# Kernel tuning notes

Hardware: AMD Instinct MI355X
Metric: run time of the kernel (lower is better)

The kernel has to match this reference:

```python
import jax, jax.numpy as jnp
import numpy as np

B, C, H, W = 4, 256, 64, 64
CQK = C // 2


def setup_inputs() -> dict:
    key = jax.random.key(0)
    ks = jax.random.split(key, 8)
    s = 0.05
    return {
        "x": jax.random.normal(ks[0], (B, C, H, W), dtype=jnp.float32),
        "wq": jax.random.normal(ks[1], (CQK, C), dtype=jnp.float32) * s,
        "bq": jax.random.normal(ks[2], (CQK,), dtype=jnp.float32) * s,
        "wk": jax.random.normal(ks[3], (CQK, C), dtype=jnp.float32) * s,
        "bk": jax.random.normal(ks[4], (CQK,), dtype=jnp.float32) * s,
        "wv": jax.random.normal(ks[5], (C, C), dtype=jnp.float32) * s,
        "bv": jax.random.normal(ks[6], (C,), dtype=jnp.float32) * s,
        "gamma": jax.random.normal(ks[7], (1,), dtype=jnp.float32),
    }


def reference(x, wq, bq, wk, bk, wv, bv, gamma):
    b, c, h, w = x.shape
    n = h * w
    xf = x.reshape(b, c, n)  # [B,C,N]
    # 1x1 convs == per-pixel linear projections
    q = jnp.einsum("oc,bcn->bon", wq, xf) + bq[:, None]  # [B,C/2,N]
    k = jnp.einsum("oc,bcn->bon", wk, xf) + bk[:, None]  # [B,C/2,N]
    v = jnp.einsum("oc,bcn->bon", wv, xf) + bv[:, None]  # [B,C,N]
    # attention[b,m,n'] = softmax_n'( sum_d q[b,d,m] * k[b,d,n'] )
    scores = jnp.einsum("bdm,bdn->bmn", q, k)  # [B,N,N]
    attn = jax.nn.softmax(scores, axis=2)
    # out_feat[b,c,j] = sum_i v[b,c,i] * attn[b,i,j]  (matmul(value, attention))
    af = jnp.einsum("bci,bij->bcj", v, attn)  # [B,C,N]
    out = gamma[0] * af.reshape(b, c, h, w) + x
    return out
```

## Files before the change

### kernel.cpp

```cpp
#include <hip/hip_runtime.h>
#include <hip/hip_bf16.h>


typedef _Float16 f16;
typedef _Float16 f16x4v __attribute__((ext_vector_type(4)));
typedef _Float16 f16x8v __attribute__((ext_vector_type(8)));
typedef float f32x4v __attribute__((ext_vector_type(4)));

static __device__ __forceinline__ f32x4v mfma16(f16x8v a, f16x8v b, f32x4v c) {
  return __builtin_amdgcn_mfma_f32_16x16x32_f16(a, b, c, 0, 0, 0);
}

#define AS1q __attribute__((address_space(1)))
#define AS3q __attribute__((address_space(3)))
static __device__ __forceinline__ void gl_lds16(const void* g, void* l) {
  __builtin_amdgcn_global_load_lds((const AS1q unsigned int*)g,
                                   (AS3q unsigned int*)l, 16, 0, 0);
}

__global__ void k_wcvt(const float* __restrict__ wq, const float* __restrict__ bq,
                       const float* __restrict__ wk, const float* __restrict__ bk,
                       const float* __restrict__ wv, const float* __restrict__ bv,
                       f16* __restrict__ wh, float* __restrict__ bcat) {
  int o = blockIdx.x;
  int c = threadIdx.x;
  const float* wrow; float bias;
  if (o < 128)      { wrow = wq + (size_t)o * 256;         bias = bq[o]; }
  else if (o < 256) { wrow = wk + (size_t)(o - 128) * 256; bias = bk[o - 128]; }
  else              { wrow = wv + (size_t)(o - 256) * 256; bias = bv[o - 256]; }
  wh[(size_t)o * 256 + c] = (f16)wrow[c];
  if (c == 0) bcat[o] = bias;
}

__global__ void k_xsplit(const float* __restrict__ x, f16* __restrict__ xh) {
  __shared__ float t[64][65];
  int b = blockIdx.z, c0 = blockIdx.y * 64, n0 = blockIdx.x * 64;
  int tx = threadIdx.x & 63, ty = threadIdx.x >> 6;
  const float* xb = x + ((size_t)b * 256 + c0) * 4096 + n0;
#pragma unroll
  for (int r = ty; r < 64; r += 4) t[r][tx] = xb[(size_t)r * 4096 + tx];
  __syncthreads();
  f16* dh = xh + ((size_t)b * 4096 + n0) * 256 + c0;
#pragma unroll
  for (int r = ty; r < 64; r += 4)
    dh[(size_t)r * 256 + tx] = (f16)t[tx][r];
}

__global__ void __launch_bounds__(256, 2)
k_proj(const f16* __restrict__ xh, const f16* __restrict__ wh,
       const float* __restrict__ bcat, f16* __restrict__ qT,
       f16* __restrict__ kT, f16* __restrict__ vT) {
  extern __shared__ char smem[];
  int b = blockIdx.z, m0 = blockIdx.y * 64, n0 = blockIdx.x * 64;
  int tid = threadIdx.x, l = tid & 63, w = tid >> 6;
  int col = l & 15, quad = l >> 4;
  const f16* Ag = xh + ((size_t)b * 4096 + m0) * 256;
  const f16* Wg = wh + (size_t)n0 * 256;
  int rloc = l >> 5;
  int l5 = l & 31;
#pragma unroll
  for (int p = 0; p < 8; p++) {
    int ci = w * 8 + p;
    int r = ci * 2 + rloc;
    int g = l5 ^ (r & 31);
    gl_lds16(Ag + (size_t)r * 256 + g * 8, smem + ci * 1024);
    gl_lds16(Wg + (size_t)r * 256 + g * 8, smem + 32768 + ci * 1024);
  }
  __syncthreads();
  const char* sA = smem;
  const char* sW = smem + 32768;
  f32x4v acc[4] = {};
  int ar = w * 16 + col;
#pragma unroll
  for (int ks = 0; ks < 8; ks++) {
    int G = ks * 4 + quad;
    f16x8v a = *(const f16x8v*)(sA + ar * 512 + ((G ^ (ar & 31)) * 16));
#pragma unroll
    for (int nt = 0; nt < 4; nt++) {
      int wr = nt * 16 + col;
      f16x8v bb = *(const f16x8v*)(sW + wr * 512 + ((G ^ (wr & 31)) * 16));
      acc[nt] = mfma16(a, bb, acc[nt]);
    }
  }
  if (n0 < 256) {
#pragma unroll
    for (int nt = 0; nt < 4; nt++) {
      int o = n0 + nt * 16 + col;
      float bias = bcat[o];
      int d = o & 127;
      f16* dst = (o < 128) ? qT : kT;
      size_t tb = (size_t)b * 524288 + (size_t)(m0 / 16 + w) * 2048 +
                  (size_t)(d >> 5) * 512 + (size_t)((d >> 3) & 3) * 128 + (d & 7);
#pragma unroll
      for (int rg = 0; rg < 4; rg++)
        dst[tb + (quad * 4 + rg) * 8] = (f16)(acc[nt][rg] + bias);
    }
  } else {
    int i2 = w * 16 + quad * 4;
    int it2 = (m0 + i2) >> 5;
    int qd2 = (i2 >> 3) & 3;
    int e2 = i2 & 7;
#pragma unroll
    for (int nt = 0; nt < 4; nt++) {
      int o = n0 + nt * 16 + col;
      float bias = bcat[o];
      int c = o - 256;
      f16x4v pv;
#pragma unroll
      for (int rg = 0; rg < 4; rg++) pv[rg] = (f16)(acc[nt][rg] + bias);
      size_t addr = (size_t)b * 1048576 + (size_t)(c >> 4) * 65536 +
                    (size_t)it2 * 512 + (size_t)qd2 * 128 + (size_t)(c & 15) * 8 + e2;
      *(f16x4v*)&vT[addr] = pv;
    }
  }
}

__global__ void __launch_bounds__(512, 2)
k_rows(const f16* __restrict__ qT, const f16* __restrict__ kT,
       float* __restrict__ partial) {
  int jblk = blockIdx.x, ih = blockIdx.y, b = blockIdx.z;
  int tid = threadIdx.x, l = tid & 63, w = tid >> 6;
  int col = l & 15;
  int ti = w & 3, jh = w >> 2;
  const f16* ktb = kT + (size_t)b * 524288 + (size_t)(jblk * 8 + jh * 4) * 2048 + l * 8;
  const f16* qtb = qT + (size_t)b * 524288 + (size_t)ti * 2048 + l * 8;
  f16x8v ka[4][4];
#pragma unroll
  for (int jt = 0; jt < 4; jt++)
#pragma unroll
    for (int ks = 0; ks < 4; ks++)
      ka[jt][ks] = *(const f16x8v*)(ktb + jt * 2048 + ks * 512);
  float* pout = partial + ((size_t)(b * 32 + jblk) * 2 + jh) * 4096 + ti * 16 + col;
  int it0 = ih * 32;
  f16x8v qfA[4], qfB[4];
#pragma unroll
  for (int ks = 0; ks < 4; ks++)
    qfA[ks] = *(const f16x8v*)(qtb + (size_t)it0 * 8192 + ks * 512);

#define ROWS_BODY(IT, QF, QN, PREF)                                           \
  {                                                                           \
    if (PREF) {                                                               \
      _Pragma("unroll") for (int ks = 0; ks < 4; ks++)                        \
        QN[ks] = *(const f16x8v*)(qtb + (size_t)((IT) + 1) * 8192 + ks * 512);\
    }                                                                         \
    f32x4v s[4] = {};                                                         \
    _Pragma("unroll") for (int ks = 0; ks < 4; ks++) {                        \
      s[0] = mfma16(ka[0][ks], QF[ks], s[0]);                                 \
      s[1] = mfma16(ka[1][ks], QF[ks], s[1]);                                 \
      s[2] = mfma16(ka[2][ks], QF[ks], s[2]);                                 \
      s[3] = mfma16(ka[3][ks], QF[ks], s[3]);                                 \
    }                                                                         \
    float t = 0.f;                                                            \
    _Pragma("unroll") for (int jt = 0; jt < 4; jt++)                          \
      _Pragma("unroll") for (int rg = 0; rg < 4; rg++)                        \
        t += __expf(s[jt][rg]);                                               \
    t += __shfl_xor(t, 16);                                                   \
    t += __shfl_xor(t, 32);                                                   \
    if (l < 16) pout[(size_t)(IT) * 64] = t;                                  \
  }

  for (int itp = 0; itp < 16; itp++) {
    int itA = it0 + itp * 2;
    ROWS_BODY(itA, qfA, qfB, true)
    ROWS_BODY(itA + 1, qfB, qfA, itp < 15)
  }
#undef ROWS_BODY
}

__global__ void k_rsum(const float* __restrict__ partial, float* __restrict__ rinv) {
  int b = blockIdx.y;
  int i = blockIdx.x * 256 + threadIdx.x;
  const float* p = partial + (size_t)b * 64 * 4096 + i;
  float s = 0.f;
#pragma unroll 8
  for (int jb = 0; jb < 64; jb++) s += p[(size_t)jb * 4096];
  rinv[(size_t)b * 4096 + i] = 1.0f / s;
}

__global__ void __launch_bounds__(512, 2)
k_fav(const f16* __restrict__ qT, const f16* __restrict__ kT,
      const f16* __restrict__ vT, const float* __restrict__ rinv,
      const float* __restrict__ x, const float* __restrict__ gamma,
      float* __restrict__ out) {
  __shared__ f16 sE[2][4096];
  int wg = blockIdx.x;
  int lg = (wg & 7) * 32 + (wg >> 3);
  int b = lg >> 6, j0 = (lg & 63) * 64;
  int tid = threadIdx.x, l = tid & 63, w = tid >> 6;
  int col = l & 15, quad = l >> 4;
  int ti = w & 3, tjb = (w >> 2) * 2;
  const f16* ktb = kT + (size_t)b * 524288 + (size_t)(j0 / 16 + tjb) * 2048 + l * 8;
  const f16* qtb = qT + (size_t)b * 524288 + (size_t)ti * 2048 + l * 8;
  const f16* vtb = vT + (size_t)b * 1048576 + (size_t)(w * 2) * 65536 + l * 8;
  const float* rp = rinv + (size_t)b * 4096 + ti * 16 + col;
  f16x8v ka0[4], ka1[4];
#pragma unroll
  for (int ks = 0; ks < 4; ks++) {
    ka0[ks] = *(const f16x8v*)(ktb + ks * 512);
    ka1[ks] = *(const f16x8v*)(ktb + 2048 + ks * 512);
  }
  f16x8v qfA[4], qfB[4], vfA[2][2], vfB[2][2];
  float rvA, rvB;
#pragma unroll
  for (int ks = 0; ks < 4; ks++) qfA[ks] = *(const f16x8v*)(qtb + ks * 512);
#pragma unroll
  for (int mt = 0; mt < 2; mt++)
#pragma unroll
    for (int ks = 0; ks < 2; ks++)
      vfA[mt][ks] = *(const f16x8v*)(vtb + mt * 65536 + ks * 512);
  rvA = rp[0];
  f32x4v acc[2][4] = {};
  int ig = ti * 2 + (col >> 3);
  int i_lo = col & 7;

#define FAV_BODY(IT, QF, VF, RV, QN, VN, RN, PREF, SEB)                        \
  {                                                                            \
    if (PREF) {                                                                \
      _Pragma("unroll") for (int ks = 0; ks < 4; ks++)                         \
        QN[ks] = *(const f16x8v*)(qtb + (size_t)((IT) + 1) * 8192 + ks * 512); \
      _Pragma("unroll") for (int mt = 0; mt < 2; mt++)                         \
        _Pragma("unroll") for (int ks = 0; ks < 2; ks++)                       \
          VN[mt][ks] = *(const f16x8v*)(vtb + mt * 65536 +                     \
                                        (size_t)(((IT) + 1) * 2 + ks) * 512);  \
      RN = rp[((IT) + 1) * 64];                                                \
    }                                                                          \
    f32x4v s0 = {}, s1 = {};                                                   \
    _Pragma("unroll") for (int ks = 0; ks < 4; ks++) {                         \
      s0 = mfma16(ka0[ks], QF[ks], s0);                                        \
      s1 = mfma16(ka1[ks], QF[ks], s1);                                        \
    }                                                                          \
    _Pragma("unroll") for (int rg = 0; rg < 4; rg++) {                         \
      int jl0 = tjb * 16 + quad * 4 + rg;                                      \
      sE[SEB][jl0 * 64 + ((ig ^ (jl0 & 7)) * 8) + i_lo] = (f16)(__expf(s0[rg]) * RV); \
      sE[SEB][(jl0 + 16) * 64 + ((ig ^ (jl0 & 7)) * 8) + i_lo] = (f16)(__expf(s1[rg]) * RV); \
    }                                                                          \
    asm volatile("s_waitcnt lgkmcnt(0)\n\ts_barrier" ::: "memory");            \
    _Pragma("unroll") for (int ks = 0; ks < 2; ks++) {                         \
      int sw = ((ks * 4 + quad) ^ (col & 7)) * 8;                              \
      f16x8v e0 = *(const f16x8v*)&sE[SEB][col * 64 + sw];                     \
      f16x8v e1 = *(const f16x8v*)&sE[SEB][(16 + col) * 64 + sw];              \
      f16x8v e2 = *(const f16x8v*)&sE[SEB][(32 + col) * 64 + sw];              \
      f16x8v e3 = *(const f16x8v*)&sE[SEB][(48 + col) * 64 + sw];              \
      acc[0][0] = mfma16(VF[0][ks], e0, acc[0][0]);                            \
      acc[0][1] = mfma16(VF[0][ks], e1, acc[0][1]);                            \
      acc[0][2] = mfma16(VF[0][ks], e2, acc[0][2]);                            \
      acc[0][3] = mfma16(VF[0][ks], e3, acc[0][3]);                            \
      acc[1][0] = mfma16(VF[1][ks], e0, acc[1][0]);                            \
      acc[1][1] = mfma16(VF[1][ks], e1, acc[1][1]);                            \
      acc[1][2] = mfma16(VF[1][ks], e2, acc[1][2]);                            \
      acc[1][3] = mfma16(VF[1][ks], e3, acc[1][3]);                            \
    }                                                                          \
  }

  for (int itp = 0; itp < 32; itp++) {
    int itA = itp * 2;
    FAV_BODY(itA, qfA, vfA, rvA, qfB, vfB, rvB, true, 0)
    FAV_BODY(itA + 1, qfB, vfB, rvB, qfA, vfA, rvA, itp < 31, 1)
  }
#undef FAV_BODY

  float gm = gamma[0];
  const float* xb = x + (size_t)b * 256 * 4096;
  float* ob = out + (size_t)b * 256 * 4096;
#pragma unroll
  for (int mt = 0; mt < 2; mt++)
#pragma unroll
    for (int jt = 0; jt < 4; jt++) {
      int c = w * 32 + mt * 16 + quad * 4;
      int j = j0 + jt * 16 + col;
#pragma unroll
      for (int rg = 0; rg < 4; rg++) {
        size_t off = (size_t)(c + rg) * 4096 + j;
        ob[off] = gm * acc[mt][jt][rg] + xb[off];
      }
    }
}

extern "C" void kernel_launch(void* const* d_in, const int* in_sizes, int n_in,
                              void* d_out, int out_size, void* d_ws, size_t ws_size,
                              hipStream_t stream) {
  (void)in_sizes; (void)n_in; (void)out_size; (void)ws_size;
  const float* x  = (const float*)d_in[0];
  const float* wq = (const float*)d_in[1];
  const float* bq = (const float*)d_in[2];
  const float* wk = (const float*)d_in[3];
  const float* bk = (const float*)d_in[4];
  const float* wv = (const float*)d_in[5];
  const float* bv = (const float*)d_in[6];
  const float* gm = (const float*)d_in[7];
  float* out = (float*)d_out;

  char* ws = (char*)d_ws;
  f16*  xh = (f16*)ws;
  f16*  qT = (f16*)(ws + 8388608);
  f16*  kT = (f16*)(ws + 12582912);
  f16*  vT = (f16*)(ws + 16777216);
  f16*  wh = (f16*)(ws + 25165824);
  float* bcat    = (float*)(ws + 25427968);
  float* rinv    = (float*)(ws + 25430016);
  float* partial = (float*)(ws + 25495552);

  hipLaunchKernelGGL(k_wcvt, dim3(512), dim3(256), 0, stream, wq, bq, wk, bk, wv, bv, wh, bcat);
  hipLaunchKernelGGL(k_xsplit, dim3(64, 4, 4), dim3(256), 0, stream, x, xh);
  hipLaunchKernelGGL(k_proj, dim3(8, 64, 4), dim3(256), 65536, stream, xh, wh, bcat, qT, kT, vT);
  hipLaunchKernelGGL(k_rows, dim3(32, 2, 4), dim3(512), 0, stream, qT, kT, partial);
  hipLaunchKernelGGL(k_rsum, dim3(16, 4), dim3(256), 0, stream, partial, rinv);
  hipLaunchKernelGGL(k_fav, dim3(256), dim3(512), 0, stream, qT, kT, vT, rinv, x, gm, out);
}
```

Baseline: 184.3 us.

## Pre-tile x and weights into MFMA fragment layout; register-resident projection GEMM

The weight-conversion and x-transpose kernels now write f16 data directly in the 16-row MFMA fragment-tiled layout, so each lane can load its operand fragments with contiguous 16-byte global loads. The projection kernel drops the LDS staging and swizzle. Each 512-thread block keeps its weight fragments in registers and loops over 8 token tiles, double-buffering the activation fragments with prefetch. This removes the LDS round-trip and reloading of weights per 64x64 tile. In exchange, the grid shrinks from 2048 to 256 blocks, and register pressure at launch bounds (512,1) is higher.

```diff
diff --git a/kernel.cpp b/kernel.cpp
--- a/kernel.cpp
+++ b/kernel.cpp
@@ -9,13 +9,6 @@
 
 static __device__ __forceinline__ f32x4v mfma16(f16x8v a, f16x8v b, f32x4v c) {
   return __builtin_amdgcn_mfma_f32_16x16x32_f16(a, b, c, 0, 0, 0);
-}
-
-#define AS1q __attribute__((address_space(1)))
-#define AS3q __attribute__((address_space(3)))
-static __device__ __forceinline__ void gl_lds16(const void* g, void* l) {
-  __builtin_amdgcn_global_load_lds((const AS1q unsigned int*)g,
-                                   (AS3q unsigned int*)l, 16, 0, 0);
 }
 
 __global__ void k_wcvt(const float* __restrict__ wq, const float* __restrict__ bq,
@@ -28,7 +21,8 @@
   if (o < 128)      { wrow = wq + (size_t)o * 256;         bias = bq[o]; }
   else if (o < 256) { wrow = wk + (size_t)(o - 128) * 256; bias = bk[o - 128]; }
   else              { wrow = wv + (size_t)(o - 256) * 256; bias = bv[o - 256]; }
-  wh[(size_t)o * 256 + c] = (f16)wrow[c];
+  wh[(size_t)(o >> 4) * 4096 + (size_t)(c >> 5) * 512 +
+     (size_t)((c >> 3) & 3) * 128 + (o & 15) * 8 + (c & 7)] = (f16)wrow[c];
   if (c == 0) bcat[o] = bias;
 }
 
@@ -40,79 +34,94 @@
 #pragma unroll
   for (int r = ty; r < 64; r += 4) t[r][tx] = xb[(size_t)r * 4096 + tx];
   __syncthreads();
-  f16* dh = xh + ((size_t)b * 4096 + n0) * 256 + c0;
-#pragma unroll
-  for (int r = ty; r < 64; r += 4)
-    dh[(size_t)r * 256 + tx] = (f16)t[tx][r];
-}
-
-__global__ void __launch_bounds__(256, 2)
+  f16* xbb = xh + (size_t)b * 1048576;
+#pragma unroll
+  for (int k2 = 0; k2 < 2; k2++) {
+    int id = k2 * 256 + threadIdx.x;
+    int tok = id & 63, oct = id >> 6;
+    int tt = n0 + tok;
+    f16x8v v;
+#pragma unroll
+    for (int e = 0; e < 8; e++) v[e] = (f16)t[oct * 8 + e][tok];
+    size_t addr = (size_t)(tt >> 4) * 4096 +
+                  (size_t)((c0 >> 5) + (oct >> 2)) * 512 +
+                  (size_t)(oct & 3) * 128 + (tt & 15) * 8;
+    *(f16x8v*)&xbb[addr] = v;
+  }
+}
+
+__global__ void __launch_bounds__(512, 1)
 k_proj(const f16* __restrict__ xh, const f16* __restrict__ wh,
        const float* __restrict__ bcat, f16* __restrict__ qT,
        f16* __restrict__ kT, f16* __restrict__ vT) {
-  extern __shared__ char smem[];
-  int b = blockIdx.z, m0 = blockIdx.y * 64, n0 = blockIdx.x * 64;
+  int ob = blockIdx.x, th = blockIdx.y, b = blockIdx.z;
   int tid = threadIdx.x, l = tid & 63, w = tid >> 6;
   int col = l & 15, quad = l >> 4;
-  const f16* Ag = xh + ((size_t)b * 4096 + m0) * 256;
-  const f16* Wg = wh + (size_t)n0 * 256;
-  int rloc = l >> 5;
-  int l5 = l & 31;
-#pragma unroll
-  for (int p = 0; p < 8; p++) {
-    int ci = w * 8 + p;
-    int r = ci * 2 + rloc;
-    int g = l5 ^ (r & 31);
-    gl_lds16(Ag + (size_t)r * 256 + g * 8, smem + ci * 1024);
-    gl_lds16(Wg + (size_t)r * 256 + g * 8, smem + 32768 + ci * 1024);
-  }
-  __syncthreads();
-  const char* sA = smem;
-  const char* sW = smem + 32768;
-  f32x4v acc[4] = {};
-  int ar = w * 16 + col;
-#pragma unroll
-  for (int ks = 0; ks < 8; ks++) {
-    int G = ks * 4 + quad;
-    f16x8v a = *(const f16x8v*)(sA + ar * 512 + ((G ^ (ar & 31)) * 16));
-#pragma unroll
-    for (int nt = 0; nt < 4; nt++) {
-      int wr = nt * 16 + col;
-      f16x8v bb = *(const f16x8v*)(sW + wr * 512 + ((G ^ (wr & 31)) * 16));
-      acc[nt] = mfma16(a, bb, acc[nt]);
-    }
-  }
-  if (n0 < 256) {
-#pragma unroll
-    for (int nt = 0; nt < 4; nt++) {
-      int o = n0 + nt * 16 + col;
-      float bias = bcat[o];
-      int d = o & 127;
-      f16* dst = (o < 128) ? qT : kT;
-      size_t tb = (size_t)b * 524288 + (size_t)(m0 / 16 + w) * 2048 +
-                  (size_t)(d >> 5) * 512 + (size_t)((d >> 3) & 3) * 128 + (d & 7);
-#pragma unroll
-      for (int rg = 0; rg < 4; rg++)
-        dst[tb + (quad * 4 + rg) * 8] = (f16)(acc[nt][rg] + bias);
-    }
-  } else {
-    int i2 = w * 16 + quad * 4;
-    int it2 = (m0 + i2) >> 5;
-    int qd2 = (i2 >> 3) & 3;
-    int e2 = i2 & 7;
-#pragma unroll
-    for (int nt = 0; nt < 4; nt++) {
-      int o = n0 + nt * 16 + col;
-      float bias = bcat[o];
-      int c = o - 256;
-      f16x4v pv;
-#pragma unroll
-      for (int rg = 0; rg < 4; rg++) pv[rg] = (f16)(acc[nt][rg] + bias);
-      size_t addr = (size_t)b * 1048576 + (size_t)(c >> 4) * 65536 +
-                    (size_t)it2 * 512 + (size_t)qd2 * 128 + (size_t)(c & 15) * 8 + e2;
-      *(f16x4v*)&vT[addr] = pv;
-    }
-  }
+  int tt = w & 3, oh = w >> 2;
+  int OT0 = ob * 4 + oh * 2;
+  const f16* wtb = wh + (size_t)OT0 * 4096 + l * 8;
+  f16x8v wb[2][8];
+#pragma unroll
+  for (int jt = 0; jt < 2; jt++)
+#pragma unroll
+    for (int ks = 0; ks < 8; ks++)
+      wb[jt][ks] = *(const f16x8v*)(wtb + jt * 4096 + ks * 512);
+  float bias0 = bcat[OT0 * 16 + col];
+  float bias1 = bcat[OT0 * 16 + 16 + col];
+  const f16* atb = xh + (size_t)b * 1048576 + (size_t)(th * 32 + tt) * 4096 + l * 8;
+  f16x8v afA[8], afB[8];
+#pragma unroll
+  for (int ks = 0; ks < 8; ks++) afA[ks] = *(const f16x8v*)(atb + ks * 512);
+
+#define PROJ_BODY(IT, AF, AN, PREF)                                            \
+  {                                                                            \
+    if (PREF) {                                                                \
+      _Pragma("unroll") for (int ks = 0; ks < 8; ks++)                         \
+        AN[ks] = *(const f16x8v*)(atb + (size_t)((IT) + 1) * 16384 + ks * 512);\
+    }                                                                          \
+    f32x4v s0 = {}, s1 = {};                                                   \
+    _Pragma("unroll") for (int ks = 0; ks < 8; ks++) {                         \
+      s0 = mfma16(AF[ks], wb[0][ks], s0);                                      \
+      s1 = mfma16(AF[ks], wb[1][ks], s1);                                      \
+    }                                                                          \
+    int T = th * 32 + (IT) * 4 + tt;                                           \
+    if (ob < 4) {                                                              \
+      f16* dst = (ob < 2) ? qT : kT;                                           \
+      _Pragma("unroll") for (int jt = 0; jt < 2; jt++) {                       \
+        int o = OT0 * 16 + jt * 16 + col;                                      \
+        int d = o & 127;                                                       \
+        float bs = jt ? bias1 : bias0;                                         \
+        size_t base = (size_t)b * 524288 + (size_t)T * 2048 +                  \
+                      (size_t)(d >> 5) * 512 + (size_t)((d >> 3) & 3) * 128 +  \
+                      (d & 7);                                                 \
+        float sv0 = jt ? s1[0] : s0[0], sv1 = jt ? s1[1] : s0[1];              \
+        float sv2 = jt ? s1[2] : s0[2], sv3 = jt ? s1[3] : s0[3];              \
+        dst[base + (quad * 4 + 0) * 8] = (f16)(sv0 + bs);                      \
+        dst[base + (quad * 4 + 1) * 8] = (f16)(sv1 + bs);                      \
+        dst[base + (quad * 4 + 2) * 8] = (f16)(sv2 + bs);                      \
+        dst[base + (quad * 4 + 3) * 8] = (f16)(sv3 + bs);                      \
+      }                                                                        \
+    } else {                                                                   \
+      int i0 = T * 16 + quad * 4;                                              \
+      size_t ibase = (size_t)b * 1048576 + (size_t)(i0 >> 5) * 512 +           \
+                     (size_t)((i0 >> 3) & 3) * 128 + (i0 & 7);                 \
+      _Pragma("unroll") for (int jt = 0; jt < 2; jt++) {                       \
+        int c = OT0 * 16 + jt * 16 + col - 256;                                \
+        float bs = jt ? bias1 : bias0;                                         \
+        f16x4v pv;                                                             \
+        _Pragma("unroll") for (int rg = 0; rg < 4; rg++)                       \
+          pv[rg] = (f16)((jt ? s1[rg] : s0[rg]) + bs);                         \
+        *(f16x4v*)&vT[ibase + (size_t)(c >> 4) * 65536 + (c & 15) * 8] = pv;   \
+      }                                                                        \
+    }                                                                          \
+  }
+
+  for (int itp = 0; itp < 4; itp++) {
+    int itA = itp * 2;
+    PROJ_BODY(itA, afA, afB, true)
+    PROJ_BODY(itA + 1, afB, afA, itp < 3)
+  }
+#undef PROJ_BODY
 }
 
 __global__ void __launch_bounds__(512, 2)
@@ -302,7 +311,7 @@
 
   hipLaunchKernelGGL(k_wcvt, dim3(512), dim3(256), 0, stream, wq, bq, wk, bk, wv, bv, wh, bcat);
   hipLaunchKernelGGL(k_xsplit, dim3(64, 4, 4), dim3(256), 0, stream, x, xh);
-  hipLaunchKernelGGL(k_proj, dim3(8, 64, 4), dim3(256), 65536, stream, xh, wh, bcat, qT, kT, vT);
+  hipLaunchKernelGGL(k_proj, dim3(8, 8, 4), dim3(512), 0, stream, xh, wh, bcat, qT, kT, vT);
   hipLaunchKernelGGL(k_rows, dim3(32, 2, 4), dim3(512), 0, stream, qT, kT, partial);
   hipLaunchKernelGGL(k_rsum, dim3(16, 4), dim3(256), 0, stream, partial, rinv);
   hipLaunchKernelGGL(k_fav, dim3(256), dim3(512), 0, stream, qT, kT, vT, rinv, x, gm, out);
```

Result: faster. 178.4 us (-3.2%).
